# Performance work log

Measured on AMD Instinct MI355X. Metric: run time of the kernel, lower is better.

The kernel has to match this reference:

```python
import jax, jax.numpy as jnp
import numpy as np

N_PHY = 12
NMUL = 4
WARM_UP = 365
NEARZERO = 1e-5
LENF = 15

# parameter_bounds order: BETA, FC, K0, K1, K2, LP, PERC, UZL, TT, CFMAX, CFR, CWH
PHY_LB = jnp.array([1.0, 50.0, 0.05, 0.01, 0.001, 0.2, 0.0, 0.0, -2.5, 0.5, 0.0, 0.0], dtype=jnp.float32)
PHY_UB = jnp.array([6.0, 1000.0, 0.9, 0.5, 0.2, 1.0, 10.0, 100.0, 2.5, 10.0, 0.1, 0.2], dtype=jnp.float32)
ROUTE_A_LB, ROUTE_A_UB = 0.0, 2.9
ROUTE_B_LB, ROUTE_B_UB = 0.0, 6.5


def _hbv_scan(p, t, pet, states, phy):
    """Run HBV step recurrence over time. p/t/pet: [T,G]; states: 5-tuple of [G,M]."""
    beta, fc, k0, k1, k2, lp, perc, uzl, tt, cfmax, cfr, cwh = phy  # each [G,M]

    def step(carry, xt):
        snowpack, meltwater, sm, suz, slz = carry
        Pt, Tt, PETt = xt
        Pt, Tt, PETt = Pt[:, None], Tt[:, None], PETt[:, None]  # [G,1] bcast vs [G,M]
        is_rain = (Tt >= tt).astype(sm.dtype)
        rain = Pt * is_rain
        snow = Pt * (1.0 - is_rain)
        snowpack = snowpack + snow
        melt = jnp.minimum(jnp.maximum(cfmax * (Tt - tt), 0.0), snowpack)
        meltwater = meltwater + melt
        snowpack = snowpack - melt
        refreeze = jnp.minimum(jnp.maximum(cfr * cfmax * (tt - Tt), 0.0), meltwater)
        snowpack = snowpack + refreeze
        meltwater = meltwater - refreeze
        tosoil = jnp.maximum(meltwater - cwh * snowpack, 0.0)
        meltwater = meltwater - tosoil
        soil_wetness = jnp.clip((sm / fc) ** beta, 0.0, 1.0)
        recharge = (rain + tosoil) * soil_wetness
        sm = sm + rain + tosoil - recharge
        excess = jnp.maximum(sm - fc, 0.0)
        sm = sm - excess
        evapfactor = jnp.clip(sm / (lp * fc), 0.0, 1.0)
        etact = jnp.minimum(sm, PETt * evapfactor)
        sm = jnp.maximum(sm - etact, NEARZERO)
        suz = suz + recharge + excess
        prc = jnp.minimum(suz, perc)
        suz = suz - prc
        q0 = k0 * jnp.maximum(suz - uzl, 0.0)
        suz = suz - q0
        q1 = k1 * suz
        suz = suz - q1
        slz = slz + prc
        q2 = k2 * slz
        slz = slz - q2
        return (snowpack, meltwater, sm, suz, slz), q0 + q1 + q2

    states, qs = jax.lax.scan(step, states, (p, t, pet))
    return qs, states  # qs: [T,G,M]


def _forward(x_phy, parameters):
    T, G, _ = x_phy.shape
    p, t, pet = x_phy[..., 0], x_phy[..., 1], x_phy[..., 2]
    # unpack physical params from last param timestep, map [0,1] -> bounds
    raw = parameters[-1, :, : N_PHY * NMUL].reshape(G, N_PHY, NMUL)
    phy_all = PHY_LB[None, :, None] + raw * (PHY_UB - PHY_LB)[None, :, None]
    phy = tuple(phy_all[:, i, :] for i in range(N_PHY))  # (beta, fc, k0, k1, k2, lp, perc, uzl, tt, cfmax, cfr, cwh)
    route = parameters[-1, :, N_PHY * NMUL :]
    a = ROUTE_A_LB + route[:, 0] * (ROUTE_A_UB - ROUTE_A_LB)
    b = ROUTE_B_LB + route[:, 1] * (ROUTE_B_UB - ROUTE_B_LB)

    s0 = jnp.full((G, NMUL), 0.001, dtype=x_phy.dtype)
    states = (s0, s0, s0, s0, s0)

    # warm-up under stop_gradient (matches torch.no_grad in original)
    phy_ng = jax.tree_util.tree_map(jax.lax.stop_gradient, phy)
    q_warm, states = _hbv_scan(
        jax.lax.stop_gradient(p[:WARM_UP]),
        jax.lax.stop_gradient(t[:WARM_UP]),
        jax.lax.stop_gradient(pet[:WARM_UP]),
        states, phy_ng)
    states = jax.tree_util.tree_map(jax.lax.stop_gradient, states)
    q_warm = jax.lax.stop_gradient(q_warm)

    q_pred, _ = _hbv_scan(p[WARM_UP:], t[WARM_UP:], pet[WARM_UP:], states, phy)
    qs = jnp.concatenate([q_warm, q_pred], axis=0).mean(-1)  # [T,G]

    # gamma unit hydrograph weights, [LENF, G]
    tg = (jnp.arange(LENF, dtype=qs.dtype) + 0.5)[:, None]
    aa = jax.nn.relu(a)[None, :] + 0.1
    th = jax.nn.relu(b)[None, :] + 0.5
    w = (tg ** (aa - 1.0)) * jnp.exp(-tg / th) / (jnp.exp(jax.scipy.special.gammaln(aa)) * th ** aa)
    w = w / w.sum(0)

    # causal depthwise (per-basin) convolution along time
    conv = jax.vmap(lambda q, u: jnp.convolve(q, u)[:T])(qs.T, w.T)  # [G,T]
    streamflow = conv.T[:, :, None]  # [T,G,1]
    return streamflow[WARM_UP:]


def setup_inputs() -> dict:
    key = jax.random.key(0)
    k1, k2, k3, k4 = jax.random.split(key, 4)
    T, G = 2000, 4000
    prcp = jax.random.uniform(k1, (T, G), dtype=jnp.float32) * 10.0   # mm/day
    tmean = jax.random.normal(k2, (T, G), dtype=jnp.float32) * 8.0    # degC
    pet = jax.random.uniform(k3, (T, G), dtype=jnp.float32) * 5.0     # mm/day
    x_phy = jnp.stack([prcp, tmean, pet], axis=-1)
    parameters = jax.random.uniform(k4, (1, G, N_PHY * NMUL + 2), dtype=jnp.float32)
    return {"x_phy": x_phy, "parameters": parameters}


def reference(x_phy, parameters):
    return _forward(x_phy, parameters)
```

## Files before the change

kernel.cpp:

```cpp
#include <hip/hip_runtime.h>

#define TT    2000
#define NG    4000
#define WARM  365
#define LENF  15
#define NPHY  12
#define BLK   30
#define SLOTW 64
#define SLOTD (BLK * SLOTW)
#define NBLK  67
#define RING  (BLK * 64)

typedef const float __attribute__((address_space(1)))* gptr_t;
typedef float __attribute__((address_space(3)))* lptr_t;

__device__ __forceinline__ float quad_sum(float x) {
    int a = __builtin_amdgcn_update_dpp(0, __float_as_int(x), 0xB1, 0xF, 0xF, true);
    float s = x + __int_as_float(a);
    int b = __builtin_amdgcn_update_dpp(0, __float_as_int(s), 0x4E, 0xF, 0xF, true);
    return s + __int_as_float(b);
}

#define WG_BARRIER() asm volatile("s_waitcnt lgkmcnt(0)\n\ts_barrier" ::: "memory")

__global__ __launch_bounds__(256, 1) void hbv_pipe_kernel(
    const float* __restrict__ xphy,
    const float* __restrict__ prm,
    float* __restrict__ out)
{
    __shared__ float s_stage[4 * SLOTD];
    __shared__ float s_rt [2 * RING];
    __shared__ float s_rex[2 * RING];
    __shared__ float s_q  [2 * RING];

    const int lane = threadIdx.x & 63;
    const int wid  = threadIdx.x >> 6;
    const int g0   = blockIdx.x * 16;
    const int g    = g0 + (lane >> 2);
    const int m    = lane & 3;

    const float* pg = prm + (size_t)g * (NPHY * 4 + 2);

    const float lb[NPHY] = {1.0f, 50.0f, 0.05f, 0.01f, 0.001f, 0.2f, 0.0f, 0.0f, -2.5f, 0.5f, 0.0f, 0.0f};
    const float ub[NPHY] = {6.0f, 1000.0f, 0.9f, 0.5f, 0.2f, 1.0f, 10.0f, 100.0f, 2.5f, 10.0f, 0.1f, 0.2f};
    float ph[NPHY];
    #pragma unroll
    for (int i = 0; i < NPHY; ++i)
        ph[i] = lb[i] + pg[i * 4 + m] * (ub[i] - lb[i]);

    const float beta = ph[0], fc = ph[1], k0 = ph[2], k1 = ph[3], k2 = ph[4],
                lp = ph[5], perc = ph[6], uzl = ph[7], ttp = ph[8],
                cfmax = ph[9], cfr = ph[10], cwh = ph[11];
    const float rfc    = 1.0f / fc;
    const float rlpfc  = 1.0f / (lp * fc);
    const float cfrcf  = cfr * cfmax;
    const float blfc   = beta * __builtin_amdgcn_logf(rfc);
    const float onemk1 = 1.0f - k1;
    const float onemk2 = 1.0f - k2;

    const float aa  = fmaxf(pg[48] * 2.9f, 0.0f) + 0.1f;
    const float th  = fmaxf(pg[49] * 6.5f, 0.0f) + 0.5f;
    const float rth = 1.0f / th;
    const float LOG2E = 1.4426950408889634f;
    float w[LENF];
    float wsum = 0.0f;
    #pragma unroll
    for (int k = 0; k < LENF; ++k) {
        const float tg = (float)k + 0.5f;
        const float e = (aa - 1.0f) * __builtin_log2f(tg) - tg * rth * LOG2E;
        w[k] = __builtin_amdgcn_exp2f(e);
        wsum += w[k];
    }
    const float rw = 0.25f / wsum;
    #pragma unroll
    for (int k = 0; k < LENF; ++k) w[k] *= rw;

    float snowpack = 0.001f, meltwater = 0.001f;
    float sm = 0.001f;
    float suz = 0.001f, slz = 0.001f;
    float qh[BLK + LENF - 1];
    #pragma unroll
    for (int d = 0; d < BLK + LENF - 1; ++d) qh[d] = 0.0f;

    const int loffd = (lane < 48 ? lane : 47);

    auto issue_blk = [&](int b) {
        const int slot = b & 3;
        const int t0 = b * BLK;
        #pragma unroll
        for (int c = 0; c < BLK; ++c) {
            int t = t0 + c;
            if (t > TT - 1) t = TT - 1;
            const float* gsrc = xphy + (size_t)t * (3 * NG) + g0 * 3 + loffd;
            float* ldst = &s_stage[slot * SLOTD + c * SLOTW];
            __builtin_amdgcn_global_load_lds((gptr_t)gsrc, (lptr_t)ldst, 4, 0, 0);
        }
    };

    if (wid == 0) { issue_blk(0); issue_blk(1); }

    for (int i = 0; i <= NBLK + 2; ++i) {
        if (wid == 0) {
            if (i < NBLK) {
                asm volatile("s_waitcnt vmcnt(30)" ::: "memory");
                issue_blk(i + 2);
                const float* sb = &s_stage[(i & 3) * SLOTD + (lane >> 2) * 3];
                float P[BLK], Tm[BLK];
                #pragma unroll
                for (int j = 0; j < BLK; ++j) { P[j] = sb[j * SLOTW]; Tm[j] = sb[j * SLOTW + 1]; }
                float* rtw = &s_rt[(i & 1) * RING + lane];
                #pragma unroll
                for (int j = 0; j < BLK; ++j) {
                    const float dT      = Tm[j] - ttp;
                    const float rain    = (Tm[j] >= ttp) ? P[j] : 0.0f;
                    const float snow    = P[j] - rain;
                    const float meltcap = cfmax * fmaxf(dT, 0.0f);
                    const float refcap  = cfrcf * fmaxf(-dT, 0.0f);
                    snowpack += snow;
                    const float melt = fminf(meltcap, snowpack);
                    meltwater += melt;
                    snowpack  -= melt;
                    const float refreeze = fminf(refcap, meltwater);
                    meltwater -= refreeze;
                    snowpack  += refreeze;
                    const float tosoil = fmaxf(fmaf(-cwh, snowpack, meltwater), 0.0f);
                    meltwater -= tosoil;
                    rtw[j * 64] = rain + tosoil;
                }
            }
        } else if (wid == 1) {
            const int b = i - 1;
            if (b >= 0 && b < NBLK) {
                const float* sb  = &s_stage[(b & 3) * SLOTD + (lane >> 2) * 3];
                const float* rtr = &s_rt[(b & 1) * RING + lane];
                float rt[BLK], ev[BLK], uum1[BLK];
                #pragma unroll
                for (int j = 0; j < BLK; ++j) { rt[j] = rtr[j * 64]; ev[j] = sb[j * SLOTW + 2]; }
                #pragma unroll
                for (int j = 0; j < BLK; ++j)
                    uum1[j] = fmaxf(fmaf(-ev[j], rlpfc, 1.0f), 0.0f);
                float* rexw = &s_rex[(b & 1) * RING + lane];
                #pragma unroll
                for (int j = 0; j < BLK; ++j) {
                    const float sw    = __builtin_amdgcn_exp2f(fmaf(beta, __builtin_amdgcn_logf(sm), blfc));
                    const float smprt = sm + rt[j];
                    const float sm1   = fmaf(-rt[j], sw, smprt);
                    const float sm2   = fminf(sm1, fc);
                    const float av = sm2 * uum1[j];
                    const float cv = sm2 - ev[j];
                    sm = fmaxf(fmaxf(av, cv), 1e-5f);
                    rexw[j * 64] = fmaf(rt[j], sw, sm1 - sm2);
                }
            }
        } else if (wid == 2) {
            const int b = i - 2;
            if (b >= 0 && b < NBLK) {
                const float* rexr = &s_rex[(b & 1) * RING + lane];
                float rex[BLK];
                #pragma unroll
                for (int j = 0; j < BLK; ++j) rex[j] = rexr[j * 64];
                float* qw = &s_q[(b & 1) * RING + lane];
                #pragma unroll
                for (int j = 0; j < BLK; ++j) {
                    const float suz1 = suz + rex[j];
                    const float prc  = fminf(suz1, perc);
                    const float suzA = suz1 - prc;
                    const float tq   = fmaxf(suzA - uzl, 0.0f);
                    const float q0   = k0 * tq;
                    const float suzB = fmaf(-k0, tq, suzA);
                    const float q1   = k1 * suzB;
                    suz = suzB * onemk1;
                    const float slz1 = slz + prc;
                    const float q2   = k2 * slz1;
                    slz = slz1 * onemk2;
                    qw[j * 64] = quad_sum(q0 + q1 + q2);
                }
            }
        } else {
            const int b = i - 3;
            if (b >= 0 && b < NBLK) {
                const int t0 = b * BLK;
                const float* qr = &s_q[(b & 1) * RING + lane];
                #pragma unroll
                for (int j = 0; j < BLK; ++j) qh[LENF - 1 + j] = qr[j * 64];
                float ov[(BLK + 3) / 4];
                #pragma unroll
                for (int k = 0; k < (BLK + 3) / 4; ++k) ov[k] = 0.0f;
                #pragma unroll
                for (int j = 0; j < BLK; ++j) {
                    float o = w[0] * qh[LENF - 1 + j];
                    #pragma unroll
                    for (int k = 1; k < LENF; ++k)
                        o = fmaf(w[k], qh[LENF - 1 + j - k], o);
                    const bool sel = ((j & 3) == m);
                    ov[j >> 2] = sel ? o : ov[j >> 2];
                }
                #pragma unroll
                for (int d = 0; d < LENF - 1; ++d) qh[d] = qh[d + BLK];
                #pragma unroll
                for (int k = 0; k < (BLK + 3) / 4; ++k) {
                    const int j = k * 4 + m;
                    const int t = t0 + j;
                    if (j < BLK && t >= WARM && t < TT)
                        out[(size_t)(t - WARM) * NG + g] = ov[k];
                }
            }
        }
        WG_BARRIER();
    }
    if (wid == 0) asm volatile("s_waitcnt vmcnt(0)" ::: "memory");
}

extern "C" void kernel_launch(void* const* d_in, const int* in_sizes, int n_in,
                              void* d_out, int out_size, void* d_ws, size_t ws_size,
                              hipStream_t stream) {
    const float* xphy = (const float*)d_in[0];
    const float* prm  = (const float*)d_in[1];
    float* out = (float*)d_out;

    hbv_pipe_kernel<<<NG / 16, 256, 0, stream>>>(xphy, prm, out);
}
```

Measured before the change: 156.3 us.

## Double pipeline block length, spread input prefetch across all waves, pack LDS handoffs

Raises the time block per pipeline stage from 30 to 60 steps, which halves the number of workgroup barriers and pipeline fill/drain iterations. Input staging moves from wave 0 alone to all four waves, each loading 15 rows into a triple-buffered slot, with a vmcnt(0) wait before every barrier. Inter-stage LDS buffers now carry float2 pairs to halve the number of LDS accesses, and stage loops read inputs inline instead of preloading arrays. The risks are a longer pipeline fill (each stage waits a whole 60-step block) and higher register pressure from the larger unrolled loops and convolution history.

```diff
diff --git a/kernel.cpp b/kernel.cpp
--- a/kernel.cpp
+++ b/kernel.cpp
@@ -5,14 +5,16 @@
 #define WARM  365
 #define LENF  15
 #define NPHY  12
-#define BLK   30
+#define BLK   60
+#define PAIRS (BLK / 2)
 #define SLOTW 64
 #define SLOTD (BLK * SLOTW)
-#define NBLK  67
-#define RING  (BLK * 64)
+#define NBLK  34
+#define ROWF  (3 * NG)
 
 typedef const float __attribute__((address_space(1)))* gptr_t;
 typedef float __attribute__((address_space(3)))* lptr_t;
+typedef __attribute__((ext_vector_type(2))) float f32x2;
 
 __device__ __forceinline__ float quad_sum(float x) {
     int a = __builtin_amdgcn_update_dpp(0, __float_as_int(x), 0xB1, 0xF, 0xF, true);
@@ -28,15 +30,16 @@
     const float* __restrict__ prm,
     float* __restrict__ out)
 {
-    __shared__ float s_stage[4 * SLOTD];
-    __shared__ float s_rt [2 * RING];
-    __shared__ float s_rex[2 * RING];
-    __shared__ float s_q  [2 * RING];
+    __shared__ float s_stage[3 * SLOTD];
+    __shared__ f32x2 s_rt [2 * PAIRS * 64];
+    __shared__ f32x2 s_rex[2 * PAIRS * 64];
+    __shared__ f32x2 s_q  [2 * PAIRS * 64];
 
     const int lane = threadIdx.x & 63;
     const int wid  = threadIdx.x >> 6;
     const int g0   = blockIdx.x * 16;
-    const int g    = g0 + (lane >> 2);
+    const int cell = lane >> 2;
+    const int g    = g0 + cell;
     const int m    = lane & 3;
 
     const float* pg = prm + (size_t)g * (NPHY * 4 + 2);
@@ -83,37 +86,55 @@
     for (int d = 0; d < BLK + LENF - 1; ++d) qh[d] = 0.0f;
 
     const int loffd = (lane < 48 ? lane : 47);
-
-    auto issue_blk = [&](int b) {
-        const int slot = b & 3;
-        const int t0 = b * BLK;
+    const float* ga = xphy + (size_t)(wid * 15) * ROWF + g0 * 3 + loffd;
+
+    {
+        float* ldst = &s_stage[(wid * 15) * SLOTW];
         #pragma unroll
-        for (int c = 0; c < BLK; ++c) {
-            int t = t0 + c;
-            if (t > TT - 1) t = TT - 1;
-            const float* gsrc = xphy + (size_t)t * (3 * NG) + g0 * 3 + loffd;
-            float* ldst = &s_stage[slot * SLOTD + c * SLOTW];
-            __builtin_amdgcn_global_load_lds((gptr_t)gsrc, (lptr_t)ldst, 4, 0, 0);
+        for (int cc = 0; cc < 15; ++cc) {
+            __builtin_amdgcn_global_load_lds((gptr_t)ga, (lptr_t)(ldst + cc * SLOTW), 4, 0, 0);
+            ga += ROWF;
         }
-    };
-
-    if (wid == 0) { issue_blk(0); issue_blk(1); }
+        ga += 45 * ROWF;
+    }
+    asm volatile("s_waitcnt vmcnt(0)" ::: "memory");
+    WG_BARRIER();
 
     for (int i = 0; i <= NBLK + 2; ++i) {
+        if (i < NBLK - 1) {
+            const int sl = (i + 1) % 3;
+            float* ldst = &s_stage[sl * SLOTD + (wid * 15) * SLOTW];
+            if (i + 1 == NBLK - 1) {
+                #pragma unroll
+                for (int cc = 0; cc < 15; ++cc) {
+                    int t = (NBLK - 1) * BLK + wid * 15 + cc;
+                    if (t > TT - 1) t = TT - 1;
+                    const float* gsrc = xphy + (size_t)t * ROWF + g0 * 3 + loffd;
+                    __builtin_amdgcn_global_load_lds((gptr_t)gsrc, (lptr_t)(ldst + cc * SLOTW), 4, 0, 0);
+                }
+            } else {
+                const float* gp2 = ga;
+                #pragma unroll
+                for (int cc = 0; cc < 15; ++cc) {
+                    __builtin_amdgcn_global_load_lds((gptr_t)gp2, (lptr_t)(ldst + cc * SLOTW), 4, 0, 0);
+                    gp2 += ROWF;
+                }
+                ga = gp2 + 45 * ROWF;
+            }
+        }
+
         if (wid == 0) {
             if (i < NBLK) {
-                asm volatile("s_waitcnt vmcnt(30)" ::: "memory");
-                issue_blk(i + 2);
-                const float* sb = &s_stage[(i & 3) * SLOTD + (lane >> 2) * 3];
-                float P[BLK], Tm[BLK];
-                #pragma unroll
-                for (int j = 0; j < BLK; ++j) { P[j] = sb[j * SLOTW]; Tm[j] = sb[j * SLOTW + 1]; }
-                float* rtw = &s_rt[(i & 1) * RING + lane];
-                #pragma unroll
-                for (int j = 0; j < BLK; ++j) {
-                    const float dT      = Tm[j] - ttp;
-                    const float rain    = (Tm[j] >= ttp) ? P[j] : 0.0f;
-                    const float snow    = P[j] - rain;
+                const float* sb = &s_stage[(i % 3) * SLOTD + cell * 3];
+                f32x2* rtw = &s_rt[(i & 1) * (PAIRS * 64) + lane];
+                float rt_even = 0.0f;
+                #pragma unroll
+                for (int j = 0; j < BLK; ++j) {
+                    const float Pt = sb[j * SLOTW];
+                    const float Tm = sb[j * SLOTW + 1];
+                    const float dT      = Tm - ttp;
+                    const float rain    = (Tm >= ttp) ? Pt : 0.0f;
+                    const float snow    = Pt - rain;
                     const float meltcap = cfmax * fmaxf(dT, 0.0f);
                     const float refcap  = cfrcf * fmaxf(-dT, 0.0f);
                     snowpack += snow;
@@ -125,44 +146,55 @@
                     snowpack  += refreeze;
                     const float tosoil = fmaxf(fmaf(-cwh, snowpack, meltwater), 0.0f);
                     meltwater -= tosoil;
-                    rtw[j * 64] = rain + tosoil;
+                    const float rt = rain + tosoil;
+                    if ((j & 1) == 0) rt_even = rt;
+                    else {
+                        f32x2 pr; pr[0] = rt_even; pr[1] = rt;
+                        rtw[(j >> 1) * 64] = pr;
+                    }
                 }
             }
         } else if (wid == 1) {
             const int b = i - 1;
             if (b >= 0 && b < NBLK) {
-                const float* sb  = &s_stage[(b & 3) * SLOTD + (lane >> 2) * 3];
-                const float* rtr = &s_rt[(b & 1) * RING + lane];
-                float rt[BLK], ev[BLK], uum1[BLK];
-                #pragma unroll
-                for (int j = 0; j < BLK; ++j) { rt[j] = rtr[j * 64]; ev[j] = sb[j * SLOTW + 2]; }
-                #pragma unroll
-                for (int j = 0; j < BLK; ++j)
-                    uum1[j] = fmaxf(fmaf(-ev[j], rlpfc, 1.0f), 0.0f);
-                float* rexw = &s_rex[(b & 1) * RING + lane];
-                #pragma unroll
-                for (int j = 0; j < BLK; ++j) {
+                const float* sb = &s_stage[(b % 3) * SLOTD + cell * 3 + 2];
+                const f32x2* rtr = &s_rt[(b & 1) * (PAIRS * 64) + lane];
+                f32x2* rexw = &s_rex[(b & 1) * (PAIRS * 64) + lane];
+                f32x2 prt; prt[0] = 0.0f; prt[1] = 0.0f;
+                float rex_even = 0.0f;
+                #pragma unroll
+                for (int j = 0; j < BLK; ++j) {
+                    if ((j & 1) == 0) prt = rtr[(j >> 1) * 64];
+                    const float rt = ((j & 1) == 0) ? prt[0] : prt[1];
+                    const float ev = sb[j * SLOTW];
                     const float sw    = __builtin_amdgcn_exp2f(fmaf(beta, __builtin_amdgcn_logf(sm), blfc));
-                    const float smprt = sm + rt[j];
-                    const float sm1   = fmaf(-rt[j], sw, smprt);
+                    const float smprt = sm + rt;
+                    const float sm1   = fmaf(-rt, sw, smprt);
                     const float sm2   = fminf(sm1, fc);
-                    const float av = sm2 * uum1[j];
-                    const float cv = sm2 - ev[j];
+                    const float uf    = fmaxf(fmaf(-ev, rlpfc, 1.0f), 0.0f);
+                    const float av    = sm2 * uf;
+                    const float cv    = sm2 - ev;
                     sm = fmaxf(fmaxf(av, cv), 1e-5f);
-                    rexw[j * 64] = fmaf(rt[j], sw, sm1 - sm2);
+                    const float rex = fmaf(rt, sw, sm1 - sm2);
+                    if ((j & 1) == 0) rex_even = rex;
+                    else {
+                        f32x2 pr; pr[0] = rex_even; pr[1] = rex;
+                        rexw[(j >> 1) * 64] = pr;
+                    }
                 }
             }
         } else if (wid == 2) {
             const int b = i - 2;
             if (b >= 0 && b < NBLK) {
-                const float* rexr = &s_rex[(b & 1) * RING + lane];
-                float rex[BLK];
-                #pragma unroll
-                for (int j = 0; j < BLK; ++j) rex[j] = rexr[j * 64];
-                float* qw = &s_q[(b & 1) * RING + lane];
-                #pragma unroll
-                for (int j = 0; j < BLK; ++j) {
-                    const float suz1 = suz + rex[j];
+                const f32x2* rexr = &s_rex[(b & 1) * (PAIRS * 64) + lane];
+                f32x2* qw = &s_q[(b & 1) * (PAIRS * 64) + lane];
+                f32x2 prx; prx[0] = 0.0f; prx[1] = 0.0f;
+                float q_even = 0.0f;
+                #pragma unroll
+                for (int j = 0; j < BLK; ++j) {
+                    if ((j & 1) == 0) prx = rexr[(j >> 1) * 64];
+                    const float rex = ((j & 1) == 0) ? prx[0] : prx[1];
+                    const float suz1 = suz + rex;
                     const float prc  = fminf(suz1, perc);
                     const float suzA = suz1 - prc;
                     const float tq   = fmaxf(suzA - uzl, 0.0f);
@@ -173,19 +205,28 @@
                     const float slz1 = slz + prc;
                     const float q2   = k2 * slz1;
                     slz = slz1 * onemk2;
-                    qw[j * 64] = quad_sum(q0 + q1 + q2);
+                    const float q = quad_sum(q0 + q1 + q2);
+                    if ((j & 1) == 0) q_even = q;
+                    else {
+                        f32x2 pr; pr[0] = q_even; pr[1] = q;
+                        qw[(j >> 1) * 64] = pr;
+                    }
                 }
             }
         } else {
             const int b = i - 3;
             if (b >= 0 && b < NBLK) {
                 const int t0 = b * BLK;
-                const float* qr = &s_q[(b & 1) * RING + lane];
-                #pragma unroll
-                for (int j = 0; j < BLK; ++j) qh[LENF - 1 + j] = qr[j * 64];
-                float ov[(BLK + 3) / 4];
-                #pragma unroll
-                for (int k = 0; k < (BLK + 3) / 4; ++k) ov[k] = 0.0f;
+                const f32x2* qr = &s_q[(b & 1) * (PAIRS * 64) + lane];
+                #pragma unroll
+                for (int jp = 0; jp < PAIRS; ++jp) {
+                    const f32x2 qp = qr[jp * 64];
+                    qh[LENF - 1 + 2 * jp]     = qp[0];
+                    qh[LENF - 1 + 2 * jp + 1] = qp[1];
+                }
+                float ov[BLK / 4];
+                #pragma unroll
+                for (int k = 0; k < BLK / 4; ++k) ov[k] = 0.0f;
                 #pragma unroll
                 for (int j = 0; j < BLK; ++j) {
                     float o = w[0] * qh[LENF - 1 + j];
@@ -198,17 +239,18 @@
                 #pragma unroll
                 for (int d = 0; d < LENF - 1; ++d) qh[d] = qh[d + BLK];
                 #pragma unroll
-                for (int k = 0; k < (BLK + 3) / 4; ++k) {
+                for (int k = 0; k < BLK / 4; ++k) {
                     const int j = k * 4 + m;
                     const int t = t0 + j;
-                    if (j < BLK && t >= WARM && t < TT)
+                    if (t >= WARM && t < TT)
                         out[(size_t)(t - WARM) * NG + g] = ov[k];
                 }
             }
         }
+
+        asm volatile("s_waitcnt vmcnt(0)" ::: "memory");
         WG_BARRIER();
     }
-    if (wid == 0) asm volatile("s_waitcnt vmcnt(0)" ::: "memory");
 }
 
 extern "C" void kernel_launch(void* const* d_in, const int* in_sizes, int n_in,
```

Result: faster. 126.8 us (-18.9%).

## Double block size, spread input staging across all waves, use rolled loops with paired LDS

Applied to the files above, without the earlier changes.

Doubles the time block to 60 steps so there are half as many pipeline stages and barriers. Input staging now uses a 3-slot ring, with every wave issuing its share of LDS loads, and each iteration waits for all loads to finish before the barrier. The stage loops are no longer fully unrolled; they run 4-step chunks with software-prefetched operands and 64-bit paired LDS reads and writes. The convolution keeps a sliding 20-value register window. Fewer barriers and lower register pressure are traded for possible exposed load latency from the full vmcnt(0) wait, and for loop overhead in the serial recurrences.

```diff
diff --git a/kernel.cpp b/kernel.cpp
--- a/kernel.cpp
+++ b/kernel.cpp
@@ -5,14 +5,16 @@
 #define WARM  365
 #define LENF  15
 #define NPHY  12
-#define BLK   30
+#define BLK   60
+#define PAIRS (BLK / 2)
 #define SLOTW 64
 #define SLOTD (BLK * SLOTW)
-#define NBLK  67
-#define RING  (BLK * 64)
+#define NBLK  34
+#define ROWF  (3 * NG)
 
 typedef const float __attribute__((address_space(1)))* gptr_t;
 typedef float __attribute__((address_space(3)))* lptr_t;
+typedef __attribute__((ext_vector_type(2))) float f32x2;
 
 __device__ __forceinline__ float quad_sum(float x) {
     int a = __builtin_amdgcn_update_dpp(0, __float_as_int(x), 0xB1, 0xF, 0xF, true);
@@ -28,15 +30,16 @@
     const float* __restrict__ prm,
     float* __restrict__ out)
 {
-    __shared__ float s_stage[4 * SLOTD];
-    __shared__ float s_rt [2 * RING];
-    __shared__ float s_rex[2 * RING];
-    __shared__ float s_q  [2 * RING];
+    __shared__ f32x2 s_rt [2 * PAIRS * 64];
+    __shared__ f32x2 s_rex[2 * PAIRS * 64];
+    __shared__ f32x2 s_q  [2 * PAIRS * 64];
+    __shared__ float s_stage[3 * SLOTD];
 
     const int lane = threadIdx.x & 63;
     const int wid  = threadIdx.x >> 6;
     const int g0   = blockIdx.x * 16;
-    const int g    = g0 + (lane >> 2);
+    const int cell = lane >> 2;
+    const int g    = g0 + cell;
     const int m    = lane & 3;
 
     const float* pg = prm + (size_t)g * (NPHY * 4 + 2);
@@ -51,10 +54,9 @@
     const float beta = ph[0], fc = ph[1], k0 = ph[2], k1 = ph[3], k2 = ph[4],
                 lp = ph[5], perc = ph[6], uzl = ph[7], ttp = ph[8],
                 cfmax = ph[9], cfr = ph[10], cwh = ph[11];
-    const float rfc    = 1.0f / fc;
     const float rlpfc  = 1.0f / (lp * fc);
     const float cfrcf  = cfr * cfmax;
-    const float blfc   = beta * __builtin_amdgcn_logf(rfc);
+    const float blfc   = beta * __builtin_amdgcn_logf(1.0f / fc);
     const float onemk1 = 1.0f - k1;
     const float onemk2 = 1.0f - k2;
 
@@ -78,137 +80,177 @@
     float snowpack = 0.001f, meltwater = 0.001f;
     float sm = 0.001f;
     float suz = 0.001f, slz = 0.001f;
-    float qh[BLK + LENF - 1];
-    #pragma unroll
-    for (int d = 0; d < BLK + LENF - 1; ++d) qh[d] = 0.0f;
+    float qw[20];
+    #pragma unroll
+    for (int d = 0; d < 20; ++d) qw[d] = 0.0f;
 
     const int loffd = (lane < 48 ? lane : 47);
 
-    auto issue_blk = [&](int b) {
-        const int slot = b & 3;
-        const int t0 = b * BLK;
-        #pragma unroll
-        for (int c = 0; c < BLK; ++c) {
-            int t = t0 + c;
-            if (t > TT - 1) t = TT - 1;
-            const float* gsrc = xphy + (size_t)t * (3 * NG) + g0 * 3 + loffd;
-            float* ldst = &s_stage[slot * SLOTD + c * SLOTW];
+    auto stage_blk = [&](int bb) {
+        const int tb = bb * BLK + wid * 15;
+        float* ldst = &s_stage[(bb % 3) * SLOTD + (wid * 15) * SLOTW];
+        #pragma unroll 1
+        for (int c = 0; c < 15; ++c) {
+            int t = tb + c; t = (t < TT) ? t : (TT - 1);
+            const float* gsrc = xphy + (size_t)t * ROWF + g0 * 3 + loffd;
             __builtin_amdgcn_global_load_lds((gptr_t)gsrc, (lptr_t)ldst, 4, 0, 0);
+            ldst += SLOTW;
         }
     };
 
-    if (wid == 0) { issue_blk(0); issue_blk(1); }
+#define SNOWSTEP(P_, T_, RT_) do {                                   \
+    const float dT_   = (T_) - ttp;                                  \
+    const float rain_ = ((T_) >= ttp) ? (P_) : 0.0f;                 \
+    const float snw_  = (P_) - rain_;                                \
+    const float mc_   = cfmax * fmaxf(dT_, 0.0f);                    \
+    const float rc_   = cfrcf * fmaxf(-dT_, 0.0f);                   \
+    snowpack += snw_;                                                \
+    const float melt_ = fminf(mc_, snowpack);                        \
+    meltwater += melt_;                                              \
+    snowpack  -= melt_;                                              \
+    const float rf_ = fminf(rc_, meltwater);                         \
+    meltwater -= rf_;                                                \
+    snowpack  += rf_;                                                \
+    const float ts_ = fmaxf(fmaf(-cwh, snowpack, meltwater), 0.0f);  \
+    meltwater -= ts_;                                                \
+    (RT_) = rain_ + ts_;                                             \
+} while (0)
+
+#define SOILSTEP(RT_, EV_, REX_) do {                                         \
+    const float sw_  = __builtin_amdgcn_exp2f(fmaf(beta, __builtin_amdgcn_logf(sm), blfc)); \
+    const float sp_  = sm + (RT_);                                            \
+    const float sm1_ = fmaf(-(RT_), sw_, sp_);                                \
+    const float sm2_ = fminf(sm1_, fc);                                       \
+    const float uf_  = fmaxf(fmaf(-(EV_), rlpfc, 1.0f), 0.0f);                \
+    sm = fmaxf(fmaxf(sm2_ * uf_, sm2_ - (EV_)), 1e-5f);                       \
+    (REX_) = fmaf((RT_), sw_, sm1_ - sm2_);                                   \
+} while (0)
+
+#define RESPSTEP(REX_, Q_) do {                                      \
+    const float s1_ = suz + (REX_);                                  \
+    const float pc_ = fminf(s1_, perc);                              \
+    const float sA_ = s1_ - pc_;                                     \
+    const float tq_ = fmaxf(sA_ - uzl, 0.0f);                        \
+    const float q0_ = k0 * tq_;                                      \
+    const float sB_ = fmaf(-k0, tq_, sA_);                           \
+    const float q1_ = k1 * sB_;                                      \
+    suz = sB_ * onemk1;                                              \
+    const float sl_ = slz + pc_;                                     \
+    const float q2_ = k2 * sl_;                                      \
+    slz = sl_ * onemk2;                                              \
+    (Q_) = quad_sum(q0_ + q1_ + q2_);                                \
+} while (0)
+
+    stage_blk(0);
+    asm volatile("s_waitcnt vmcnt(0)" ::: "memory");
+    WG_BARRIER();
 
     for (int i = 0; i <= NBLK + 2; ++i) {
+        if (i < NBLK - 1) stage_blk(i + 1);
+
         if (wid == 0) {
             if (i < NBLK) {
-                asm volatile("s_waitcnt vmcnt(30)" ::: "memory");
-                issue_blk(i + 2);
-                const float* sb = &s_stage[(i & 3) * SLOTD + (lane >> 2) * 3];
-                float P[BLK], Tm[BLK];
-                #pragma unroll
-                for (int j = 0; j < BLK; ++j) { P[j] = sb[j * SLOTW]; Tm[j] = sb[j * SLOTW + 1]; }
-                float* rtw = &s_rt[(i & 1) * RING + lane];
-                #pragma unroll
-                for (int j = 0; j < BLK; ++j) {
-                    const float dT      = Tm[j] - ttp;
-                    const float rain    = (Tm[j] >= ttp) ? P[j] : 0.0f;
-                    const float snow    = P[j] - rain;
-                    const float meltcap = cfmax * fmaxf(dT, 0.0f);
-                    const float refcap  = cfrcf * fmaxf(-dT, 0.0f);
-                    snowpack += snow;
-                    const float melt = fminf(meltcap, snowpack);
-                    meltwater += melt;
-                    snowpack  -= melt;
-                    const float refreeze = fminf(refcap, meltwater);
-                    meltwater -= refreeze;
-                    snowpack  += refreeze;
-                    const float tosoil = fmaxf(fmaf(-cwh, snowpack, meltwater), 0.0f);
-                    meltwater -= tosoil;
-                    rtw[j * 64] = rain + tosoil;
+                const float* sb = &s_stage[(i % 3) * SLOTD + cell * 3];
+                f32x2* rtw = &s_rt[(i & 1) * (PAIRS * 64) + lane];
+                float P0 = sb[0], T0 = sb[1], P1 = sb[SLOTW], T1 = sb[SLOTW + 1],
+                      P2 = sb[2 * SLOTW], T2 = sb[2 * SLOTW + 1],
+                      P3 = sb[3 * SLOTW], T3 = sb[3 * SLOTW + 1];
+                sb += 4 * SLOTW;
+                #pragma unroll 1
+                for (int ch = 0; ch < BLK / 4; ++ch) {
+                    const float nP0 = sb[0], nT0 = sb[1], nP1 = sb[SLOTW], nT1 = sb[SLOTW + 1],
+                                nP2 = sb[2 * SLOTW], nT2 = sb[2 * SLOTW + 1],
+                                nP3 = sb[3 * SLOTW], nT3 = sb[3 * SLOTW + 1];
+                    sb += 4 * SLOTW;
+                    float r0, r1, r2, r3;
+                    SNOWSTEP(P0, T0, r0); SNOWSTEP(P1, T1, r1);
+                    SNOWSTEP(P2, T2, r2); SNOWSTEP(P3, T3, r3);
+                    f32x2 a; a[0] = r0; a[1] = r1; rtw[0] = a;
+                    f32x2 b; b[0] = r2; b[1] = r3; rtw[64] = b;
+                    rtw += 128;
+                    P0 = nP0; T0 = nT0; P1 = nP1; T1 = nT1;
+                    P2 = nP2; T2 = nT2; P3 = nP3; T3 = nT3;
                 }
             }
         } else if (wid == 1) {
             const int b = i - 1;
             if (b >= 0 && b < NBLK) {
-                const float* sb  = &s_stage[(b & 3) * SLOTD + (lane >> 2) * 3];
-                const float* rtr = &s_rt[(b & 1) * RING + lane];
-                float rt[BLK], ev[BLK], uum1[BLK];
-                #pragma unroll
-                for (int j = 0; j < BLK; ++j) { rt[j] = rtr[j * 64]; ev[j] = sb[j * SLOTW + 2]; }
-                #pragma unroll
-                for (int j = 0; j < BLK; ++j)
-                    uum1[j] = fmaxf(fmaf(-ev[j], rlpfc, 1.0f), 0.0f);
-                float* rexw = &s_rex[(b & 1) * RING + lane];
-                #pragma unroll
-                for (int j = 0; j < BLK; ++j) {
-                    const float sw    = __builtin_amdgcn_exp2f(fmaf(beta, __builtin_amdgcn_logf(sm), blfc));
-                    const float smprt = sm + rt[j];
-                    const float sm1   = fmaf(-rt[j], sw, smprt);
-                    const float sm2   = fminf(sm1, fc);
-                    const float av = sm2 * uum1[j];
-                    const float cv = sm2 - ev[j];
-                    sm = fmaxf(fmaxf(av, cv), 1e-5f);
-                    rexw[j * 64] = fmaf(rt[j], sw, sm1 - sm2);
+                const float* sbe = &s_stage[(b % 3) * SLOTD + cell * 3 + 2];
+                const f32x2* rtr = &s_rt[(b & 1) * (PAIRS * 64) + lane];
+                f32x2* rexw = &s_rex[(b & 1) * (PAIRS * 64) + lane];
+                f32x2 rA = rtr[0], rB = rtr[64];
+                float e0 = sbe[0], e1 = sbe[SLOTW], e2 = sbe[2 * SLOTW], e3 = sbe[3 * SLOTW];
+                rtr += 128; sbe += 4 * SLOTW;
+                #pragma unroll 1
+                for (int ch = 0; ch < BLK / 4; ++ch) {
+                    const f32x2 nA = rtr[0], nB = rtr[64];
+                    const float ne0 = sbe[0], ne1 = sbe[SLOTW],
+                                ne2 = sbe[2 * SLOTW], ne3 = sbe[3 * SLOTW];
+                    rtr += 128; sbe += 4 * SLOTW;
+                    float x0, x1, x2, x3;
+                    SOILSTEP(rA[0], e0, x0); SOILSTEP(rA[1], e1, x1);
+                    SOILSTEP(rB[0], e2, x2); SOILSTEP(rB[1], e3, x3);
+                    f32x2 a; a[0] = x0; a[1] = x1; rexw[0] = a;
+                    f32x2 b2; b2[0] = x2; b2[1] = x3; rexw[64] = b2;
+                    rexw += 128;
+                    rA = nA; rB = nB; e0 = ne0; e1 = ne1; e2 = ne2; e3 = ne3;
                 }
             }
         } else if (wid == 2) {
             const int b = i - 2;
             if (b >= 0 && b < NBLK) {
-                const float* rexr = &s_rex[(b & 1) * RING + lane];
-                float rex[BLK];
-                #pragma unroll
-                for (int j = 0; j < BLK; ++j) rex[j] = rexr[j * 64];
-                float* qw = &s_q[(b & 1) * RING + lane];
-                #pragma unroll
-                for (int j = 0; j < BLK; ++j) {
-                    const float suz1 = suz + rex[j];
-                    const float prc  = fminf(suz1, perc);
-                    const float suzA = suz1 - prc;
-                    const float tq   = fmaxf(suzA - uzl, 0.0f);
-                    const float q0   = k0 * tq;
-                    const float suzB = fmaf(-k0, tq, suzA);
-                    const float q1   = k1 * suzB;
-                    suz = suzB * onemk1;
-                    const float slz1 = slz + prc;
-                    const float q2   = k2 * slz1;
-                    slz = slz1 * onemk2;
-                    qw[j * 64] = quad_sum(q0 + q1 + q2);
+                const f32x2* rexr = &s_rex[(b & 1) * (PAIRS * 64) + lane];
+                f32x2* qwr = &s_q[(b & 1) * (PAIRS * 64) + lane];
+                f32x2 rA = rexr[0], rB = rexr[64];
+                rexr += 128;
+                #pragma unroll 1
+                for (int ch = 0; ch < BLK / 4; ++ch) {
+                    const f32x2 nA = rexr[0], nB = rexr[64];
+                    rexr += 128;
+                    float q0, q1, q2, q3;
+                    RESPSTEP(rA[0], q0); RESPSTEP(rA[1], q1);
+                    RESPSTEP(rB[0], q2); RESPSTEP(rB[1], q3);
+                    f32x2 a; a[0] = q0; a[1] = q1; qwr[0] = a;
+                    f32x2 b2; b2[0] = q2; b2[1] = q3; qwr[64] = b2;
+                    qwr += 128;
+                    rA = nA; rB = nB;
                 }
             }
         } else {
             const int b = i - 3;
             if (b >= 0 && b < NBLK) {
                 const int t0 = b * BLK;
-                const float* qr = &s_q[(b & 1) * RING + lane];
-                #pragma unroll
-                for (int j = 0; j < BLK; ++j) qh[LENF - 1 + j] = qr[j * 64];
-                float ov[(BLK + 3) / 4];
-                #pragma unroll
-                for (int k = 0; k < (BLK + 3) / 4; ++k) ov[k] = 0.0f;
-                #pragma unroll
-                for (int j = 0; j < BLK; ++j) {
-                    float o = w[0] * qh[LENF - 1 + j];
+                const f32x2* qr = &s_q[(b & 1) * (PAIRS * 64) + lane];
+                f32x2 c0 = qr[0], c1 = qr[64], c2 = qr[128];
+                qr += 192;
+                #pragma unroll 1
+                for (int ch = 0; ch < BLK / 6; ++ch) {
+                    const f32x2 n0 = qr[0], n1 = qr[64], n2 = qr[128];
+                    qr += 192;
                     #pragma unroll
-                    for (int k = 1; k < LENF; ++k)
-                        o = fmaf(w[k], qh[LENF - 1 + j - k], o);
-                    const bool sel = ((j & 3) == m);
-                    ov[j >> 2] = sel ? o : ov[j >> 2];
-                }
-                #pragma unroll
-                for (int d = 0; d < LENF - 1; ++d) qh[d] = qh[d + BLK];
-                #pragma unroll
-                for (int k = 0; k < (BLK + 3) / 4; ++k) {
-                    const int j = k * 4 + m;
-                    const int t = t0 + j;
-                    if (j < BLK && t >= WARM && t < TT)
-                        out[(size_t)(t - WARM) * NG + g] = ov[k];
+                    for (int d = 0; d < 14; ++d) qw[d] = qw[d + 6];
+                    qw[14] = c0[0]; qw[15] = c0[1]; qw[16] = c1[0];
+                    qw[17] = c1[1]; qw[18] = c2[0]; qw[19] = c2[1];
+                    const int jb = ch * 6;
+                    #pragma unroll
+                    for (int c = 0; c < 6; ++c) {
+                        float o = w[0] * qw[14 + c];
+                        #pragma unroll
+                        for (int k = 1; k < LENF; ++k)
+                            o = fmaf(w[k], qw[14 + c - k], o);
+                        const int j = jb + c;
+                        const int t = t0 + j;
+                        if (((j & 3) == m) && t >= WARM && t < TT)
+                            out[(size_t)(t - WARM) * NG + g] = o;
+                    }
+                    c0 = n0; c1 = n1; c2 = n2;
                 }
             }
         }
+
+        asm volatile("s_waitcnt vmcnt(0)" ::: "memory");
         WG_BARRIER();
     }
-    if (wid == 0) asm volatile("s_waitcnt vmcnt(0)" ::: "memory");
 }
 
 extern "C" void kernel_launch(void* const* d_in, const int* in_sizes, int n_in,
```

After: 185.6 us. 1.19x slower.
